# Optimization experiments

Hardware: AMD Instinct MI355X
Metric: run time of the kernel (lower is better)

The kernel has to match this reference:

```python
import jax, jax.numpy as jnp
import numpy as np

B, V, T, FIN = 32, 512, 12, 2      # batch, num_nodes, seq_len, input_dim
DG, CH, HOR = 20, 16, 12           # dgraphs, channels, horizon
KS, EPS, RF = 2, 0.3, 13           # kernel_size, FAGCN eps, receptive field
DILS = (1, 2, 1, 2, 1, 2, 1, 2)    # blocks=4, layers=2 -> dilations per layer
NL = len(DILS)
BN_EPS = 1e-5


def conv2d(x, W, b, dil=1):
    # x: [B,Cin,V,T], W: [Cout,Cin,1,k] -> [B,Cout,V,T'] (VALID, time-dilated)
    y = jax.lax.conv_general_dilated(x, W, (1, 1), 'VALID',
                                     rhs_dilation=(1, dil),
                                     dimension_numbers=('NCHW', 'OIHW', 'NCHW'))
    return y + b[None, :, None, None]


def setup_inputs():
    key = jax.random.key(0)
    ks = jax.random.split(key, 12)
    w = lambda k, s: jax.random.normal(k, s, dtype=jnp.float32) * 0.05
    z = lambda s: jnp.zeros(s, dtype=jnp.float32)
    o = lambda s: jnp.ones(s, dtype=jnp.float32)
    return {
        'input': jax.random.normal(ks[0], (T, B, V, FIN), dtype=jnp.float32),
        'start_W': w(ks[1], (CH, FIN, 1, 1)), 'start_b': z((CH,)),
        'filt_W': w(ks[2], (NL, CH, CH, 1, KS)), 'filt_b': z((NL, CH)),
        'gate_W': w(ks[3], (NL, CH, CH, 1, KS)), 'gate_b': z((NL, CH)),
        'skip_W': w(ks[4], (NL, CH, CH, 1, 1)), 'skip_b': z((NL, CH)),
        'gconv_W': w(ks[5], (NL, CH, 4 * CH, 1, 1)), 'gconv_b': z((NL, CH)),
        'bn_gamma': o((NL, CH)), 'bn_beta': z((NL, CH)),
        'bn_mean': z((NL, CH)), 'bn_var': o((NL, CH)),
        'end1_W': w(ks[6], (CH, CH, 1, 1)), 'end1_b': z((CH,)),
        'end2_W': w(ks[7], (HOR, CH, 1, 1)), 'end2_b': z((HOR,)),
        'lin_W': w(ks[8], (DG, FIN * T)), 'lin_b': z((DG,)),
        'fc1_W': w(ks[9], (V, DG)), 'fc1_b': z((V,)),
        'fc2_W': w(ks[10], (V, DG)), 'fc2_b': z((V,)),
        'fc3_W': w(ks[11], (V, DG)), 'fc3_b': z((V,)),
    }


def reference(input, start_W, start_b, filt_W, filt_b, gate_W, gate_b,
              skip_W, skip_b, gconv_W, gconv_b, bn_gamma, bn_beta, bn_mean,
              bn_var, end1_W, end1_b, end2_W, end2_b, lin_W, lin_b,
              fc1_W, fc1_b, fc2_W, fc2_b, fc3_W, fc3_b):
    x_in = jnp.transpose(input, (1, 3, 2, 0))            # [B,FIN,V,T]
    # ---- Instant_graph / SpectralConv1d: FFT-based graph learner ----
    xr = jnp.transpose(x_in, (0, 2, 3, 1)).reshape(B, V, T * FIN)
    ff = jnp.fft.fft(xr, axis=-1)                        # complex64 [B,V,T*FIN]
    real = ff.real @ lin_W.T + lin_b                     # [B,V,DG]
    img = ff.imag @ lin_W.T + lin_b                      # [B,V,DG]
    iff = jnp.fft.irfft(real + 1j * img, n=V, axis=1)    # [B,V,DG]
    Am = jnp.sqrt(real * real + img * img)
    S = jnp.arctan(real / (img + 1e-4))
    mid = jax.nn.sigmoid((iff @ fc1_W.T + fc1_b + Am @ fc2_W.T + fc2_b
                          + S @ fc3_W.T + fc3_b) / 3.0)  # [B,V,V]
    adj = jax.nn.sigmoid(jnp.mean(mid, axis=0))          # [V,V]
    eye = jnp.eye(V, dtype=x_in.dtype)
    Lm = EPS * eye + adj
    Hm = EPS * eye - adj
    # ---- WaveNet-style trunk with FAGCN diffusion per layer ----
    x = jnp.pad(x_in, ((0, 0), (0, 0), (0, 0), (RF - T, 0)))
    x = conv2d(x, start_W, start_b)                      # [B,CH,V,RF]
    skip = None
    for i in range(NL):
        residual = x
        f = jnp.tanh(conv2d(x, filt_W[i], filt_b[i], DILS[i]))
        g = jax.nn.sigmoid(conv2d(x, gate_W[i], gate_b[i], DILS[i]))
        x = f * g
        s = conv2d(x, skip_W[i], skip_b[i])
        skip = s if skip is None else s + skip[..., -s.shape[3]:]
        # FAGCN order=2: concat [xL, xLL, xH, xHH] on channels -> 1x1 conv
        outs = []
        for a in (Lm, Hm):
            x1 = jnp.einsum('ncvl,vw->ncwl', x, a)
            outs.append(x1)
            outs.append(jnp.einsum('ncvl,vw->ncwl', x1, a))
        h = conv2d(jnp.concatenate(outs, axis=1), gconv_W[i], gconv_b[i])
        x = h + residual[..., -h.shape[3]:]
        # BatchNorm2d (eval mode / running stats)
        x = ((x - bn_mean[i][None, :, None, None])
             / jnp.sqrt(bn_var[i][None, :, None, None] + BN_EPS)
             * bn_gamma[i][None, :, None, None]
             + bn_beta[i][None, :, None, None])
    out = jax.nn.relu(skip)
    out = jax.nn.relu(conv2d(out, end1_W, end1_b))
    out = conv2d(out, end2_W, end2_b)                    # [B,HOR,V,1]
    return out, adj
```

## Files before the change

kernel.cpp:

```cpp
#include <hip/hip_runtime.h>
#include <hip/hip_bf16.h>

using bf16 = __hip_bfloat16;
typedef unsigned short ushort_t;
typedef float f32x4 __attribute__((ext_vector_type(4)));
typedef short bf16x8 __attribute__((ext_vector_type(8)));

__device__ __forceinline__ float tof(bf16 x) { return __bfloat162float(x); }
__device__ __forceinline__ float tofu(ushort_t u) { return __uint_as_float((unsigned)u << 16); }
__device__ __forceinline__ ushort_t f2bf(float x) {
  unsigned u = __float_as_uint(x);
  return (ushort_t)((u + 0x7FFF + ((u >> 16) & 1)) >> 16);
}
__device__ __forceinline__ float sigm(float x) { return 1.f / (1.f + __expf(-x)); }
__device__ __forceinline__ float tanh_fast(float x) {
  float e2 = __expf(2.f * x);
  return 1.f - 2.f / (e2 + 1.f);
}

#define B_ 32
#define V_ 512
#define EPS_ 0.3f

constexpr size_t OFF_C    = 1024;
constexpr size_t OFF_S    = 1504;
constexpr size_t OFF_WEFF = 1984;
constexpr size_t OFF_R    = 8128;
constexpr size_t OFF_I    = 335808;
constexpr size_t OFF_G    = 663488;
constexpr size_t OFF_BTHI = 663488;
constexpr size_t OFF_BTLO = 925632;
constexpr size_t OFF_ADJ  = 1712064;
constexpr size_t OFF_ADJ2 = 1974208;
constexpr size_t OFF_SKIP = 2236352;
constexpr size_t OFF_X0   = 2498496;
constexpr size_t OFF_X1   = 5906368;
constexpr size_t OFF_TBH  = 5906368;
constexpr size_t OFF_TBL  = 6045632;
constexpr size_t OFF_TAH  = 6184896;
constexpr size_t OFF_TAL  = 6358976;
constexpr size_t OFF_UHI  = 9314240;
constexpr size_t OFF_ULO  = 10887104;
constexpr size_t OFF_PADJ = 12722112;
constexpr size_t OFF_WCT  = 13770688;
constexpr size_t OFF_FLAG = 19013568;
constexpr size_t OFF_CIN  = 19013576;
constexpr size_t WS_TOTAL = 19459584;

__global__ __launch_bounds__(256) void k_detect(const void* __restrict__ in0,
                                                float* __restrict__ flag) {
  __shared__ int cnt;
  if (threadIdx.x == 0) cnt = 0;
  __syncthreads();
  const unsigned short* u = (const unsigned short*)in0;
  int bad = 0;
  for (int i = threadIdx.x; i < 4096; i += 256) {
    int e = (u[i] >> 7) & 0xFF;
    if (e == 255 || (e != 0 && (e < 87 || e > 167))) bad++;
  }
  atomicAdd(&cnt, bad);
  __syncthreads();
  if (threadIdx.x == 0) flag[0] = (cnt > 200) ? 1.f : 0.f;
}

struct P26 { const void* p[26]; };
__global__ __launch_bounds__(256) void k_convall(const void* __restrict__ in0, P26 ps,
                                                 float* __restrict__ dstin,
                                                 float* __restrict__ dstw,
                                                 const float* __restrict__ flag) {
  int tid = threadIdx.x;
  if (blockIdx.x < 384) {
    int i4 = blockIdx.x * 256 + tid;
    if (flag[0] > 0.5f) {
      ((float4*)dstin)[i4] = ((const float4*)in0)[i4];
    } else {
      ushort4 v = ((const ushort4*)in0)[i4];
      dstin[i4 * 4 + 0] = tofu(v.x);
      dstin[i4 * 4 + 1] = tofu(v.y);
      dstin[i4 * 4 + 2] = tofu(v.z);
      dstin[i4 * 4 + 3] = tofu(v.w);
    }
  } else {
    const int sz[26] = {32, 16, 4096, 128, 4096, 128, 2048, 128, 8192, 128,
                        128, 128, 128, 128, 256, 16, 192, 12, 480, 20,
                        10240, 512, 10240, 512, 10240, 512};
    int gid = (blockIdx.x - 384) * 256 + tid;
    if (gid >= 52736) return;
    int s = 0, off = 0;
    while (gid >= off + sz[s]) { off += sz[s]; ++s; }
    int local = gid - off;
    float v = (flag[0] > 0.5f) ? ((const float*)ps.p[s])[local]
                               : tofu(((const ushort_t*)ps.p[s])[local]);
    dstw[gid] = v;
  }
}

__global__ __launch_bounds__(256) void k_pre(const float* __restrict__ linW,
                                             const float* __restrict__ gconvW,
                                             const float* f1W, const float* f1b,
                                             const float* f2W, const float* f2b,
                                             const float* f3W, const float* f3b,
                                             float* __restrict__ ws) {
  int idx = blockIdx.x * 256 + threadIdx.x;
  const float TWO_PI = 6.2831853071795864769f;
  if (idx < 512) {
  } else if (idx < 992) {
    int e = idx - 512, d = e / 24, n = e % 24;
    float c = 0.f, s = 0.f;
    for (int k = 0; k < 24; ++k) {
      int j = (k * n) % 24;
      float ang = TWO_PI * (float)j / 24.f;
      float w = linW[d * 24 + k];
      c += w * cosf(ang);
      s -= w * sinf(ang);
    }
    ws[OFF_C + e] = c;
    ws[OFF_S + e] = s;
  } else if (idx < 3040) {
    int e = idx - 992, i = e >> 8, co = (e >> 4) & 15, ci = e & 15;
    size_t base = (size_t)(i * 16 + co) * 64 + ci;
    float W0 = gconvW[base];
    float W1 = gconvW[base + 16];
    float W2 = gconvW[base + 32];
    float W3 = gconvW[base + 48];
    size_t o = OFF_WEFF + (size_t)i * 768 + co * 16 + ci;
    ws[o]       = EPS_ * (W0 + W2) + EPS_ * EPS_ * (W1 + W3);
    ws[o + 256] = (W0 - W2) + 2.f * EPS_ * (W1 - W3);
    ws[o + 512] = W1 + W3;
  } else if (idx < 36320) {
    int e = idx - 3040;
    if (e < 32768) {
      int k = e >> 9, w = e & 511;
      float v = 0.f;
      if (k < 20) v = f1W[w * 20 + k];
      else if (k < 40) v = f2W[w * 20 + k - 20];
      else if (k < 60) v = f3W[w * 20 + k - 40];
      ws[OFF_WCT + e] = v;
    } else {
      int w = e - 32768;
      ws[OFF_WCT + e] = f1b[w] + f2b[w] + f3b[w];
    }
  } else if (idx < 36320 + 278528) {
    int e = idx - 36320;
    int m = e / 544, kk = e - m * 544;
    float val = 0.f;
    if (kk < 514) {
      int k = kk >> 1;
      int j = (k * m) & 511;
      float ang = TWO_PI * (float)j * (1.f / 512.f);
      val = ((kk & 1) ? sinf(ang) : cosf(ang)) * (1.f / 512.f);
    }
    ushort_t h = f2bf(val);
    float hf = tofu(h);
    ((ushort_t*)(ws + OFF_TBH))[e] = h;
    ((ushort_t*)(ws + OFF_TBL))[e] = f2bf(val - hf);
  }
}

__global__ __launch_bounds__(256) void k_fft(const float* __restrict__ in,
                                             const float* __restrict__ linb,
                                             const float* __restrict__ ws,
                                             float* __restrict__ Rw, float* __restrict__ Iw,
                                             float* __restrict__ G) {
  __shared__ float Cl[480], Sl[480], lb[20];
  int tid = threadIdx.x;
  for (int e = tid; e < 480; e += 256) { Cl[e] = ws[OFF_C + e]; Sl[e] = ws[OFF_S + e]; }
  if (tid < 20) lb[tid] = linb[tid];
  __syncthreads();
  int gid = blockIdx.x * 256 + tid;
  int b = gid >> 9, v = gid & 511;
  float xr[24];
#pragma unroll
  for (int t = 0; t < 12; ++t) {
    size_t ib = (((size_t)t * 32 + b) * 512 + v) * 2;
    xr[2 * t] = in[ib];
    xr[2 * t + 1] = in[ib + 1];
  }
  size_t gbv = (size_t)b * 512 + v;
  for (int d = 0; d < 20; ++d) {
    float R = lb[d], I = lb[d];
#pragma unroll
    for (int n = 0; n < 24; ++n) {
      R = fmaf(xr[n], Cl[d * 24 + n], R);
      I = fmaf(xr[n], Sl[d * 24 + n], I);
    }
    Rw[gbv * 20 + d] = R;
    Iw[gbv * 20 + d] = I;
    G[gbv * 64 + 20 + d] = sqrtf(R * R + I * I);
    G[gbv * 64 + 40 + d] = atanf(R / (I + 1e-4f));
  }
  G[gbv * 64 + 60] = 0.f; G[gbv * 64 + 61] = 0.f;
  G[gbv * 64 + 62] = 0.f; G[gbv * 64 + 63] = 0.f;
}

__global__ __launch_bounds__(256) void k_irprep(const float* __restrict__ Rw,
                                                const float* __restrict__ Iw,
                                                ushort_t* __restrict__ Ahi,
                                                ushort_t* __restrict__ Alo) {
  int e = blockIdx.x * 256 + threadIdx.x;
  if (e >= 348160) return;
  int row = e / 544, kk = e - row * 544;
  int b = row / 20, d = row - b * 20;
  float val = 0.f;
  if (kk < 514) {
    int k = kk >> 1;
    float ck = (k == 0 || k == 256) ? 1.f : 2.f;
    size_t src = ((size_t)b * 512 + k) * 20 + d;
    val = (kk & 1) ? (-ck * Iw[src]) : (ck * Rw[src]);
  }
  ushort_t h = f2bf(val);
  Ahi[e] = h;
  Alo[e] = f2bf(val - tofu(h));
}

__global__ __launch_bounds__(512) void k_irgemm(const ushort_t* __restrict__ Ah_g,
                                                const ushort_t* __restrict__ Al_g,
                                                const ushort_t* __restrict__ Bh_g,
                                                const ushort_t* __restrict__ Bl_g,
                                                float* __restrict__ G) {
  __shared__ ushort_t Ah[128 * 40], Al[128 * 40], Bh[64 * 40], Bl[64 * 40];
  int tid = threadIdx.x;
  int lane = tid & 63, wv = tid >> 6;
  int quad = lane >> 4, l15 = lane & 15;
  int wr = wv >> 1, wc = wv & 1;
  int m0 = blockIdx.x * 128;
  int nv0 = blockIdx.y * 64;
  int srow = tid >> 2, seg = tid & 3;
  size_t baseA = (size_t)(m0 + srow) * 544 + seg * 8;
  size_t baseB = (size_t)(nv0 + (srow & 63)) * 544 + seg * 8;
  int slo = srow * 40 + seg * 8;
  uint4 pAh = *(const uint4*)&Ah_g[baseA];
  uint4 pAl = *(const uint4*)&Al_g[baseA];
  uint4 pBh, pBl;
  if (tid < 256) { pBh = *(const uint4*)&Bh_g[baseB]; pBl = *(const uint4*)&Bl_g[baseB]; }
  f32x4 acc[2][2] = {};
  for (int kt = 0; kt < 17; ++kt) {
    *(uint4*)&Ah[slo] = pAh;
    *(uint4*)&Al[slo] = pAl;
    if (tid < 256) { *(uint4*)&Bh[slo] = pBh; *(uint4*)&Bl[slo] = pBl; }
    __syncthreads();
    if (kt < 16) {
      int ko = (kt + 1) * 32;
      pAh = *(const uint4*)&Ah_g[baseA + ko];
      pAl = *(const uint4*)&Al_g[baseA + ko];
      if (tid < 256) { pBh = *(const uint4*)&Bh_g[baseB + ko]; pBl = *(const uint4*)&Bl_g[baseB + ko]; }
    }
    bf16x8 afh[2], afl[2], bfh[2], bfl[2];
#pragma unroll
    for (int i = 0; i < 2; ++i) {
      int mr = (wr * 32 + i * 16 + l15) * 40 + quad * 8;
      afh[i] = *(const bf16x8*)&Ah[mr];
      afl[i] = *(const bf16x8*)&Al[mr];
    }
#pragma unroll
    for (int j = 0; j < 2; ++j) {
      int nr = (wc * 32 + j * 16 + l15) * 40 + quad * 8;
      bfh[j] = *(const bf16x8*)&Bh[nr];
      bfl[j] = *(const bf16x8*)&Bl[nr];
    }
#pragma unroll
    for (int i = 0; i < 2; ++i)
#pragma unroll
      for (int j = 0; j < 2; ++j) {
        acc[i][j] = __builtin_amdgcn_mfma_f32_16x16x32_bf16(afh[i], bfh[j], acc[i][j], 0, 0, 0);
        acc[i][j] = __builtin_amdgcn_mfma_f32_16x16x32_bf16(afh[i], bfl[j], acc[i][j], 0, 0, 0);
        acc[i][j] = __builtin_amdgcn_mfma_f32_16x16x32_bf16(afl[i], bfh[j], acc[i][j], 0, 0, 0);
      }
    __syncthreads();
  }
#pragma unroll
  for (int i = 0; i < 2; ++i)
#pragma unroll
    for (int j = 0; j < 2; ++j)
#pragma unroll
      for (int r = 0; r < 4; ++r) {
        int arow = m0 + wr * 32 + i * 16 + quad * 4 + r;
        int col = nv0 + wc * 32 + j * 16 + l15;
        int b = arow / 20, d = arow - b * 20;
        G[((size_t)b * 512 + col) * 64 + d] = acc[i][j][r];
      }
}

__global__ __launch_bounds__(256) void k_adj(const float* __restrict__ G,
                                             const float* __restrict__ wct,
                                             float* __restrict__ padj) {
  __shared__ float As[64 * 68], Bs[64 * 68], bsl[64];
  int tid = threadIdx.x, tx = tid & 15, ty = tid >> 4;
  int w0 = blockIdx.x * 64, m0 = blockIdx.y * 64, z = blockIdx.z;
  for (int i = 0; i < 16; ++i) {
    int idx = tid + i * 256;
    Bs[(idx >> 6) * 68 + (idx & 63)] = wct[(size_t)(idx >> 6) * 512 + w0 + (idx & 63)];
  }
  if (tid < 64) bsl[tid] = wct[32768 + w0 + tid];
  float sum[4][4] = {};
  for (int bi = 0; bi < 8; ++bi) {
    int bb = z * 8 + bi;
    __syncthreads();
    for (int i = 0; i < 4; ++i) {
      int idx = tid + i * 256;
      int row = idx >> 4, seg = idx & 15;
      float4 g = *(const float4*)&G[((size_t)bb * 512 + m0 + row) * 64 + seg * 4];
      As[(seg * 4 + 0) * 68 + row] = g.x;
      As[(seg * 4 + 1) * 68 + row] = g.y;
      As[(seg * 4 + 2) * 68 + row] = g.z;
      As[(seg * 4 + 3) * 68 + row] = g.w;
    }
    __syncthreads();
    float dot[4][4] = {};
    for (int kk = 0; kk < 64; ++kk) {
      float4 a = *(const float4*)&As[kk * 68 + ty * 4];
      float4 b = *(const float4*)&Bs[kk * 68 + tx * 4];
      float ar[4] = {a.x, a.y, a.z, a.w}, br[4] = {b.x, b.y, b.z, b.w};
#pragma unroll
      for (int r = 0; r < 4; ++r)
#pragma unroll
        for (int c = 0; c < 4; ++c) dot[r][c] = fmaf(ar[r], br[c], dot[r][c]);
    }
#pragma unroll
    for (int r = 0; r < 4; ++r)
#pragma unroll
      for (int c = 0; c < 4; ++c)
        sum[r][c] += sigm((dot[r][c] + bsl[tx * 4 + c]) * (1.f / 3.f));
  }
  float* pz = padj + (size_t)z * 262144;
#pragma unroll
  for (int r = 0; r < 4; ++r)
#pragma unroll
    for (int c = 0; c < 4; ++c)
      pz[(size_t)(m0 + ty * 4 + r) * 512 + w0 + tx * 4 + c] = sum[r][c];
}

__global__ __launch_bounds__(256) void k_adjfin(const float* __restrict__ padj,
                                                float* __restrict__ adjw,
                                                void* __restrict__ outp,
                                                const float* __restrict__ flag) {
  int idx = blockIdx.x * 256 + threadIdx.x;
  float s = padj[idx] + padj[idx + 262144] + padj[idx + 524288] + padj[idx + 786432];
  float a = sigm(s * (1.f / 32.f));
  adjw[idx] = a;
  if (flag[0] > 0.5f) ((float*)outp)[196608 + idx] = a;
  else ((ushort_t*)outp)[196608 + idx] = f2bf(a);
}

__global__ __launch_bounds__(256) void k_gemm(const float* __restrict__ A,
                                              const float* __restrict__ B0,
                                              const float* __restrict__ B1,
                                              float* __restrict__ C, int ldc) {
  __shared__ float As[32][68];
  __shared__ float Bs[32][68];
  int bx = blockIdx.x, by = blockIdx.y;
  const float* __restrict__ Bp = (bx < 8) ? B0 : B1;
  int n0 = (bx & 7) * 64, m0 = by * 64;
  int tid = threadIdx.x, tx = tid & 15, ty = tid >> 4;
  float acc[4][4] = {};
  for (int kb = 0; kb < 512; kb += 32) {
#pragma unroll
    for (int s = 0; s < 2; ++s) {
      int f = tid + s * 256;
      int row = f >> 3, k4 = (f & 7) << 2;
      float4 a4 = *(const float4*)(A + (size_t)(m0 + row) * 512 + kb + k4);
      As[k4 + 0][row] = a4.x;
      As[k4 + 1][row] = a4.y;
      As[k4 + 2][row] = a4.z;
      As[k4 + 3][row] = a4.w;
      int kk = f >> 4, c4 = (f & 15) << 2;
      *(float4*)&Bs[kk][c4] = *(const float4*)(Bp + (size_t)(kb + kk) * 512 + n0 + c4);
    }
    __syncthreads();
#pragma unroll
    for (int kk = 0; kk < 32; ++kk) {
      float4 a = *(const float4*)&As[kk][ty << 2];
      float4 b = *(const float4*)&Bs[kk][tx << 2];
      float ar[4] = {a.x, a.y, a.z, a.w}, br[4] = {b.x, b.y, b.z, b.w};
#pragma unroll
      for (int r = 0; r < 4; ++r)
#pragma unroll
        for (int c = 0; c < 4; ++c) acc[r][c] = fmaf(ar[r], br[c], acc[r][c]);
    }
    __syncthreads();
  }
#pragma unroll
  for (int r = 0; r < 4; ++r) {
    float4 o = make_float4(acc[r][0], acc[r][1], acc[r][2], acc[r][3]);
    *(float4*)(C + (size_t)(m0 + (ty << 2) + r) * ldc + bx * 64 + (tx << 2)) = o;
  }
}

__global__ __launch_bounds__(256) void k_splitB(const float* __restrict__ adjw,
                                                const float* __restrict__ adj2w,
                                                ushort_t* __restrict__ Bh,
                                                ushort_t* __restrict__ Bl) {
  __shared__ float til[32][33];
  int tid = threadIdx.x;
  int k0 = blockIdx.x * 32;
  int nb = blockIdx.y;
  const float* src = (nb < 16) ? adjw : adj2w;
  int ns = (nb * 32) & 511;
  for (int i = 0; i < 4; ++i) {
    int idx = tid + i * 256;
    int r = idx >> 5, c = idx & 31;
    til[r][c] = src[(size_t)(k0 + r) * 512 + ns + c];
  }
  __syncthreads();
  for (int i = 0; i < 4; ++i) {
    int idx = tid + i * 256;
    int rr = idx >> 5, cc = idx & 31;
    float v = til[cc][rr];
    ushort_t h = f2bf(v);
    float hf = tofu(h);
    ushort_t l = f2bf(v - hf);
    size_t o = (size_t)(nb * 32 + rr) * 512 + k0 + cc;
    Bh[o] = h;
    Bl[o] = l;
  }
}

__global__ __launch_bounds__(256) void k_start(const float* __restrict__ in,
                                               const float* __restrict__ stW,
                                               const float* __restrict__ stb,
                                               float* __restrict__ X0) {
  __shared__ float w[32], bl[16];
  int tid = threadIdx.x;
  if (tid < 32) w[tid] = stW[tid];
  if (tid < 16) bl[tid] = stb[tid];
  __syncthreads();
  int blk = blockIdx.x;
  int b = blk / 26, rem = blk % 26, t = rem >> 1, v = (rem & 1) * 256 + tid;
  float f0 = 0.f, f1 = 0.f;
  if (t > 0) {
    size_t ib = (((size_t)(t - 1) * 32 + b) * 512 + v) * 2;
    f0 = in[ib];
    f1 = in[ib + 1];
  }
#pragma unroll
  for (int c = 0; c < 16; ++c)
    X0[((size_t)(b * 13 + t) * 16 + c) * 512 + v] = fmaf(w[c * 2], f0, fmaf(w[c * 2 + 1], f1, bl[c]));
}

__global__ __launch_bounds__(256) void k_gate(const float* __restrict__ X,
                                              ushort_t* __restrict__ Uhi,
                                              ushort_t* __restrict__ Ulo,
                                              float* __restrict__ skip,
                                              const float* fW, const float* fb,
                                              const float* gW, const float* gb,
                                              const float* sW, const float* sb,
                                              int i, int L, int Lo, int d) {
  __shared__ float wf[512], wg[512], swl[256], fbl[16], gbl[16], sbl[16];
  int tid = threadIdx.x;
  for (int e = tid; e < 512; e += 256) { wf[e] = fW[i * 512 + e]; wg[e] = gW[i * 512 + e]; }
  if (tid < 256) swl[tid] = sW[i * 256 + tid];
  if (tid < 16) { fbl[tid] = fb[i * 16 + tid]; gbl[tid] = gb[i * 16 + tid]; sbl[tid] = sb[i * 16 + tid]; }
  __syncthreads();
  int blk = blockIdx.x;
  int b = blk / (2 * Lo), rem = blk % (2 * Lo), t = rem >> 1, v = (rem & 1) * 256 + tid;
  float x0[16], x1[16];
  size_t base0 = (size_t)(b * L + t) * 16 * 512 + v;
  size_t base1 = (size_t)(b * L + t + d) * 16 * 512 + v;
#pragma unroll
  for (int ci = 0; ci < 16; ++ci) { x0[ci] = X[base0 + ci * 512]; x1[ci] = X[base1 + ci * 512]; }
  float u[16];
#pragma unroll
  for (int co = 0; co < 16; ++co) {
    float f = fbl[co], g = gbl[co];
#pragma unroll
    for (int ci = 0; ci < 16; ++ci) {
      f = fmaf(wf[co * 32 + ci * 2], x0[ci], f);
      f = fmaf(wf[co * 32 + ci * 2 + 1], x1[ci], f);
      g = fmaf(wg[co * 32 + ci * 2], x0[ci], g);
      g = fmaf(wg[co * 32 + ci * 2 + 1], x1[ci], g);
    }
    float uu = tanh_fast(f) * sigm(g);
    u[co] = uu;
    ushort_t h = f2bf(uu);
    float hf = tofu(h);
    ushort_t l = f2bf(uu - hf);
    size_t o = ((size_t)(b * Lo + t) * 16 + co) * 512 + v;
    Uhi[o] = h;
    Ulo[o] = l;
  }
  if (t == Lo - 1) {
#pragma unroll
    for (int c = 0; c < 16; ++c) {
      float s = sbl[c];
#pragma unroll
      for (int ci = 0; ci < 16; ++ci) s = fmaf(swl[c * 16 + ci], u[ci], s);
      skip[((size_t)b * 16 + c) * 512 + v] += s;
    }
  }
}

__global__ __launch_bounds__(512) void k_mfmac(const ushort_t* __restrict__ Uhi,
                                               const ushort_t* __restrict__ Ulo,
                                               const ushort_t* __restrict__ Bh_g,
                                               const ushort_t* __restrict__ Bl_g,
                                               const float* __restrict__ Xres,
                                               float* __restrict__ Xn,
                                               const float* __restrict__ ws,
                                               const float* gcb, const float* bg,
                                               const float* bb2, const float* bm,
                                               const float* bv,
                                               int li, int L, int Lo, int d) {
  __shared__ __align__(16) char smem[40960];
  ushort_t* Ah = (ushort_t*)smem;
  ushort_t* Al = Ah + 5120;
  ushort_t* Bh = Al + 5120;
  ushort_t* Bl = Bh + 5120;
  float* yt = (float*)smem;
  __shared__ float wx[256], wy1[256], wy2[256], gbl[16], bsc[16], bsh[16];
  int tid = threadIdx.x;
  const float* we = ws + OFF_WEFF + (size_t)li * 768;
  if (tid < 256) { wx[tid] = we[tid]; wy1[tid] = we[256 + tid]; wy2[tid] = we[512 + tid]; }
  if (tid < 16) {
    gbl[tid] = gcb[li * 16 + tid];
    float sc = bg[li * 16 + tid] * rsqrtf(bv[li * 16 + tid] + 1e-5f);
    bsc[tid] = sc;
    bsh[tid] = bb2[li * 16 + tid] - bm[li * 16 + tid] * sc;
  }
  int lane = tid & 63, wv = tid >> 6;
  int quad = lane >> 4, l15 = lane & 15;
  int wr = wv >> 1, wc = wv & 1;
  int m0 = blockIdx.x * 128;
  int nv0 = blockIdx.y * 64;
  int srow = tid >> 2, seg = tid & 3;
  size_t baseA = ((size_t)(m0 + srow)) * 512 + seg * 8;
  int brow = (srow < 64) ? (nv0 + srow) : (448 + nv0 + srow);
  size_t baseB = ((size_t)brow) * 512 + seg * 8;
  int slo = srow * 40 + seg * 8;
  uint4 pAh = *(const uint4*)&Uhi[baseA];
  uint4 pAl = *(const uint4*)&Ulo[baseA];
  uint4 pBh = *(const uint4*)&Bh_g[baseB];
  uint4 pBl = *(const uint4*)&Bl_g[baseB];
  f32x4 acc[2][4] = {};
  for (int kt = 0; kt < 16; ++kt) {
    *(uint4*)&Ah[slo] = pAh;
    *(uint4*)&Al[slo] = pAl;
    *(uint4*)&Bh[slo] = pBh;
    *(uint4*)&Bl[slo] = pBl;
    __syncthreads();
    if (kt < 15) {
      int ko = (kt + 1) * 32;
      pAh = *(const uint4*)&Uhi[baseA + ko];
      pAl = *(const uint4*)&Ulo[baseA + ko];
      pBh = *(const uint4*)&Bh_g[baseB + ko];
      pBl = *(const uint4*)&Bl_g[baseB + ko];
    }
    bf16x8 afh[2], afl[2], bfh[4], bfl[4];
#pragma unroll
    for (int i = 0; i < 2; ++i) {
      int mr = (wr * 32 + i * 16 + l15) * 40 + quad * 8;
      afh[i] = *(const bf16x8*)&Ah[mr];
      afl[i] = *(const bf16x8*)&Al[mr];
    }
#pragma unroll
    for (int j = 0; j < 4; ++j) {
      int nr = (wc * 64 + j * 16 + l15) * 40 + quad * 8;
      bfh[j] = *(const bf16x8*)&Bh[nr];
      bfl[j] = *(const bf16x8*)&Bl[nr];
    }
#pragma unroll
    for (int i = 0; i < 2; ++i)
#pragma unroll
      for (int j = 0; j < 4; ++j) {
        acc[i][j] = __builtin_amdgcn_mfma_f32_16x16x32_bf16(afh[i], bfh[j], acc[i][j], 0, 0, 0);
        acc[i][j] = __builtin_amdgcn_mfma_f32_16x16x32_bf16(afh[i], bfl[j], acc[i][j], 0, 0, 0);
        acc[i][j] = __builtin_amdgcn_mfma_f32_16x16x32_bf16(afl[i], bfh[j], acc[i][j], 0, 0, 0);
      }
    __syncthreads();
  }
  int g = tid >> 5, lv = tid & 31;
  int gg = (m0 >> 4) + g;
  int b = gg / Lo, t = gg - b * Lo;
  size_t rb = (size_t)gg * 16;
  size_t resb = ((size_t)(b * L + t + d) * 16) * 512;
#pragma unroll
  for (int p = 0; p < 2; ++p) {
#pragma unroll
    for (int i = 0; i < 2; ++i)
#pragma unroll
      for (int jj = 0; jj < 2; ++jj) {
        int j = p * 2 + jj;
#pragma unroll
        for (int r = 0; r < 4; ++r) {
          int row = wr * 32 + i * 16 + quad * 4 + r;
          int col = jj * 16 + l15 + 32 * wc;
          yt[row * 66 + col] = acc[i][j][r];
        }
      }
    __syncthreads();
    if (tid < 256) {
      int v = nv0 + p * 32 + lv;
      float uu[16], z1[16], z2[16];
#pragma unroll
      for (int ci = 0; ci < 16; ++ci) {
        size_t o = (rb + ci) * 512 + v;
        uu[ci] = tofu(Uhi[o]) + tofu(Ulo[o]);
        z1[ci] = yt[(g * 16 + ci) * 66 + lv];
        z2[ci] = yt[(g * 16 + ci) * 66 + 32 + lv];
      }
#pragma unroll
      for (int co = 0; co < 16; ++co) {
        float h = gbl[co];
#pragma unroll
        for (int ci = 0; ci < 16; ++ci) {
          h = fmaf(wx[co * 16 + ci], uu[ci], h);
          h = fmaf(wy1[co * 16 + ci], z1[ci], h);
          h = fmaf(wy2[co * 16 + ci], z2[ci], h);
        }
        float val = h + Xres[resb + co * 512 + v];
        val = fmaf(val, bsc[co], bsh[co]);
        Xn[(rb + co) * 512 + v] = val;
      }
    }
    if (p == 0) __syncthreads();
  }
}

__global__ __launch_bounds__(256) void k_end(const float* __restrict__ skip,
                                             const float* e1W, const float* e1b,
                                             const float* e2W, const float* e2b,
                                             void* __restrict__ outp,
                                             const float* __restrict__ flag) {
  __shared__ float w1[256], b1[16], w2[192], b2[12];
  int tid = threadIdx.x;
  if (tid < 256) w1[tid] = e1W[tid];
  if (tid < 192) w2[tid] = e2W[tid];
  if (tid < 16) b1[tid] = e1b[tid];
  if (tid < 12) b2[tid] = e2b[tid];
  __syncthreads();
  float isf32 = flag[0];
  int gid = blockIdx.x * 256 + tid;
  int b = gid >> 9, v = gid & 511;
  float sk[16], e1[16];
#pragma unroll
  for (int ci = 0; ci < 16; ++ci) sk[ci] = fmaxf(skip[((size_t)b * 16 + ci) * 512 + v], 0.f);
#pragma unroll
  for (int c = 0; c < 16; ++c) {
    float a = b1[c];
#pragma unroll
    for (int ci = 0; ci < 16; ++ci) a = fmaf(w1[c * 16 + ci], sk[ci], a);
    e1[c] = fmaxf(a, 0.f);
  }
#pragma unroll
  for (int h = 0; h < 12; ++h) {
    float o = b2[h];
#pragma unroll
    for (int ci = 0; ci < 16; ++ci) o = fmaf(w2[h * 16 + ci], e1[ci], o);
    size_t oi = ((size_t)b * 12 + h) * 512 + v;
    if (isf32 > 0.5f) ((float*)outp)[oi] = o;
    else ((ushort_t*)outp)[oi] = f2bf(o);
  }
}

extern "C" void kernel_launch(void* const* d_in, const int* in_sizes, int n_in,
                              void* d_out, int out_size, void* d_ws, size_t ws_size,
                              hipStream_t stream) {
  float* ws = (float*)d_ws;
  if (ws_size < WS_TOTAL * sizeof(float)) return;

  static const int CSZ[27] = {393216, 32, 16, 4096, 128, 4096, 128, 2048, 128, 8192, 128,
                              128, 128, 128, 128, 256, 16, 192, 12, 480, 20,
                              10240, 512, 10240, 512, 10240, 512};
  float* cv[27];
  {
    size_t off = OFF_CIN;
    for (int i = 0; i < 27; ++i) { cv[i] = ws + off; off += (size_t)CSZ[i]; }
  }
  float* flag = ws + OFF_FLAG;

  k_detect<<<1, 256, 0, stream>>>(d_in[0], flag);
  P26 ps;
  for (int i = 0; i < 26; ++i) ps.p[i] = d_in[i + 1];
  k_convall<<<590, 256, 0, stream>>>(d_in[0], ps, cv[0], cv[1], flag);

  const float* IN = cv[0];
  const float* stW = cv[1];  const float* stb = cv[2];
  const float* fW = cv[3];   const float* fb = cv[4];
  const float* gW = cv[5];   const float* gb = cv[6];
  const float* sW = cv[7];   const float* sb = cv[8];
  const float* gcW = cv[9];  const float* gcb = cv[10];
  const float* bng = cv[11]; const float* bnb = cv[12];
  const float* bnm = cv[13]; const float* bnv = cv[14];
  const float* e1W = cv[15]; const float* e1b = cv[16];
  const float* e2W = cv[17]; const float* e2b = cv[18];
  const float* linW = cv[19]; const float* linb = cv[20];
  const float* f1W = cv[21]; const float* f1b = cv[22];
  const float* f2W = cv[23]; const float* f2b = cv[24];
  const float* f3W = cv[25]; const float* f3b = cv[26];

  hipMemsetAsync(ws + OFF_SKIP, 0, (size_t)B_ * 16 * V_ * sizeof(float), stream);
  k_pre<<<1230, 256, 0, stream>>>(linW, gcW, f1W, f1b, f2W, f2b, f3W, f3b, ws);
  k_fft<<<64, 256, 0, stream>>>(IN, linb, ws, ws + OFF_R, ws + OFF_I, ws + OFF_G);
  k_irprep<<<1360, 256, 0, stream>>>(ws + OFF_R, ws + OFF_I,
                                     (ushort_t*)(ws + OFF_TAH), (ushort_t*)(ws + OFF_TAL));
  k_irgemm<<<dim3(5, 8), 512, 0, stream>>>((ushort_t*)(ws + OFF_TAH), (ushort_t*)(ws + OFF_TAL),
                                           (ushort_t*)(ws + OFF_TBH), (ushort_t*)(ws + OFF_TBL),
                                           ws + OFF_G);
  k_adj<<<dim3(8, 8, 4), 256, 0, stream>>>(ws + OFF_G, ws + OFF_WCT, ws + OFF_PADJ);
  k_adjfin<<<1024, 256, 0, stream>>>(ws + OFF_PADJ, ws + OFF_ADJ, d_out, flag);
  k_gemm<<<dim3(8, 8), 256, 0, stream>>>(ws + OFF_ADJ, ws + OFF_ADJ, ws + OFF_ADJ,
                                         ws + OFF_ADJ2, 512);
  k_splitB<<<dim3(16, 32), 256, 0, stream>>>(ws + OFF_ADJ, ws + OFF_ADJ2,
                                             (ushort_t*)(ws + OFF_BTHI),
                                             (ushort_t*)(ws + OFF_BTLO));
  k_start<<<832, 256, 0, stream>>>(IN, stW, stb, ws + OFF_X0);

  float* cur = ws + OFF_X0;
  float* nxt = ws + OFF_X1;
  ushort_t* UHI = (ushort_t*)(ws + OFF_UHI);
  ushort_t* ULO = (ushort_t*)(ws + OFF_ULO);
  int L = 13;
  const int dils[8] = {1, 2, 1, 2, 1, 2, 1, 2};
  for (int i = 0; i < 8; ++i) {
    int d = dils[i], Lo = L - d;
    k_gate<<<64 * Lo, 256, 0, stream>>>(cur, UHI, ULO, ws + OFF_SKIP,
                                        fW, fb, gW, gb, sW, sb, i, L, Lo, d);
    k_mfmac<<<dim3(4 * Lo, 8), 512, 0, stream>>>(UHI, ULO,
                                                 (ushort_t*)(ws + OFF_BTHI),
                                                 (ushort_t*)(ws + OFF_BTLO),
                                                 cur, nxt, ws,
                                                 gcb, bng, bnb, bnm, bnv, i, L, Lo, d);
    float* tmp = cur; cur = nxt; nxt = tmp;
    L = Lo;
  }
  k_end<<<64, 256, 0, stream>>>(ws + OFF_SKIP, e1W, e1b, e2W, e2b, d_out, flag);
}
```

Before: 594.7 us.

## Load MFMA fragments directly from global memory, drop LDS staging in graph GEMM

The split-bf16 graph-propagation GEMM no longer stages A/B tiles through shared memory with per-k-step barriers. Each wave now loads its MFMA operand fragments straight from global memory into registers, with one-step register prefetch. The block shrinks to 256 threads covering 32 nodes, and the grid doubles in y so the epilogue runs in a single pass. This removes LDS traffic and barriers, but duplicates global loads across waves that share B tiles, relying on cache for reuse.

```diff
diff --git a/kernel.cpp b/kernel.cpp
--- a/kernel.cpp
+++ b/kernel.cpp
@@ -489,7 +489,7 @@
   }
 }
 
-__global__ __launch_bounds__(512) void k_mfmac(const ushort_t* __restrict__ Uhi,
+__global__ __launch_bounds__(256) void k_mfmac(const ushort_t* __restrict__ Uhi,
                                                const ushort_t* __restrict__ Ulo,
                                                const ushort_t* __restrict__ Bh_g,
                                                const ushort_t* __restrict__ Bl_g,
@@ -500,118 +500,104 @@
                                                const float* bb2, const float* bm,
                                                const float* bv,
                                                int li, int L, int Lo, int d) {
-  __shared__ __align__(16) char smem[40960];
-  ushort_t* Ah = (ushort_t*)smem;
-  ushort_t* Al = Ah + 5120;
-  ushort_t* Bh = Al + 5120;
-  ushort_t* Bl = Bh + 5120;
-  float* yt = (float*)smem;
+  __shared__ float yt[128 * 66];
   __shared__ float wx[256], wy1[256], wy2[256], gbl[16], bsc[16], bsh[16];
   int tid = threadIdx.x;
   const float* we = ws + OFF_WEFF + (size_t)li * 768;
-  if (tid < 256) { wx[tid] = we[tid]; wy1[tid] = we[256 + tid]; wy2[tid] = we[512 + tid]; }
+  wx[tid] = we[tid]; wy1[tid] = we[256 + tid]; wy2[tid] = we[512 + tid];
   if (tid < 16) {
     gbl[tid] = gcb[li * 16 + tid];
     float sc = bg[li * 16 + tid] * rsqrtf(bv[li * 16 + tid] + 1e-5f);
     bsc[tid] = sc;
     bsh[tid] = bb2[li * 16 + tid] - bm[li * 16 + tid] * sc;
   }
-  int lane = tid & 63, wv = tid >> 6;
+  int lane = tid & 63, wr = tid >> 6;
   int quad = lane >> 4, l15 = lane & 15;
-  int wr = wv >> 1, wc = wv & 1;
   int m0 = blockIdx.x * 128;
-  int nv0 = blockIdx.y * 64;
-  int srow = tid >> 2, seg = tid & 3;
-  size_t baseA = ((size_t)(m0 + srow)) * 512 + seg * 8;
-  int brow = (srow < 64) ? (nv0 + srow) : (448 + nv0 + srow);
-  size_t baseB = ((size_t)brow) * 512 + seg * 8;
-  int slo = srow * 40 + seg * 8;
-  uint4 pAh = *(const uint4*)&Uhi[baseA];
-  uint4 pAl = *(const uint4*)&Ulo[baseA];
-  uint4 pBh = *(const uint4*)&Bh_g[baseB];
-  uint4 pBl = *(const uint4*)&Bl_g[baseB];
+  int nv0 = blockIdx.y * 32;
+  size_t aoff[2], boff[4];
+#pragma unroll
+  for (int i = 0; i < 2; ++i)
+    aoff[i] = (size_t)(m0 + wr * 32 + i * 16 + l15) * 512 + quad * 8;
+  boff[0] = (size_t)(nv0 + l15) * 512 + quad * 8;
+  boff[1] = boff[0] + 16 * 512;
+  boff[2] = boff[0] + 512 * 512;
+  boff[3] = boff[1] + 512 * 512;
+  bf16x8 cAh[2], cAl[2], cBh[4], cBl[4];
+#pragma unroll
+  for (int i = 0; i < 2; ++i) {
+    cAh[i] = *(const bf16x8*)&Uhi[aoff[i]];
+    cAl[i] = *(const bf16x8*)&Ulo[aoff[i]];
+  }
+#pragma unroll
+  for (int j = 0; j < 4; ++j) {
+    cBh[j] = *(const bf16x8*)&Bh_g[boff[j]];
+    cBl[j] = *(const bf16x8*)&Bl_g[boff[j]];
+  }
   f32x4 acc[2][4] = {};
   for (int kt = 0; kt < 16; ++kt) {
-    *(uint4*)&Ah[slo] = pAh;
-    *(uint4*)&Al[slo] = pAl;
-    *(uint4*)&Bh[slo] = pBh;
-    *(uint4*)&Bl[slo] = pBl;
-    __syncthreads();
-    if (kt < 15) {
-      int ko = (kt + 1) * 32;
-      pAh = *(const uint4*)&Uhi[baseA + ko];
-      pAl = *(const uint4*)&Ulo[baseA + ko];
-      pBh = *(const uint4*)&Bh_g[baseB + ko];
-      pBl = *(const uint4*)&Bl_g[baseB + ko];
-    }
-    bf16x8 afh[2], afl[2], bfh[4], bfl[4];
+    int ko = ((kt + 1) & 15) * 32;
+    bf16x8 nAh[2], nAl[2], nBh[4], nBl[4];
 #pragma unroll
     for (int i = 0; i < 2; ++i) {
-      int mr = (wr * 32 + i * 16 + l15) * 40 + quad * 8;
-      afh[i] = *(const bf16x8*)&Ah[mr];
-      afl[i] = *(const bf16x8*)&Al[mr];
+      nAh[i] = *(const bf16x8*)&Uhi[aoff[i] + ko];
+      nAl[i] = *(const bf16x8*)&Ulo[aoff[i] + ko];
     }
 #pragma unroll
     for (int j = 0; j < 4; ++j) {
-      int nr = (wc * 64 + j * 16 + l15) * 40 + quad * 8;
-      bfh[j] = *(const bf16x8*)&Bh[nr];
-      bfl[j] = *(const bf16x8*)&Bl[nr];
+      nBh[j] = *(const bf16x8*)&Bh_g[boff[j] + ko];
+      nBl[j] = *(const bf16x8*)&Bl_g[boff[j] + ko];
     }
 #pragma unroll
     for (int i = 0; i < 2; ++i)
 #pragma unroll
       for (int j = 0; j < 4; ++j) {
-        acc[i][j] = __builtin_amdgcn_mfma_f32_16x16x32_bf16(afh[i], bfh[j], acc[i][j], 0, 0, 0);
-        acc[i][j] = __builtin_amdgcn_mfma_f32_16x16x32_bf16(afh[i], bfl[j], acc[i][j], 0, 0, 0);
-        acc[i][j] = __builtin_amdgcn_mfma_f32_16x16x32_bf16(afl[i], bfh[j], acc[i][j], 0, 0, 0);
+        acc[i][j] = __builtin_amdgcn_mfma_f32_16x16x32_bf16(cAh[i], cBh[j], acc[i][j], 0, 0, 0);
+        acc[i][j] = __builtin_amdgcn_mfma_f32_16x16x32_bf16(cAh[i], cBl[j], acc[i][j], 0, 0, 0);
+        acc[i][j] = __builtin_amdgcn_mfma_f32_16x16x32_bf16(cAl[i], cBh[j], acc[i][j], 0, 0, 0);
       }
-    __syncthreads();
-  }
+#pragma unroll
+    for (int i = 0; i < 2; ++i) { cAh[i] = nAh[i]; cAl[i] = nAl[i]; }
+#pragma unroll
+    for (int j = 0; j < 4; ++j) { cBh[j] = nBh[j]; cBl[j] = nBl[j]; }
+  }
+#pragma unroll
+  for (int i = 0; i < 2; ++i)
+#pragma unroll
+    for (int j = 0; j < 4; ++j)
+#pragma unroll
+      for (int r = 0; r < 4; ++r) {
+        int row = wr * 32 + i * 16 + quad * 4 + r;
+        int col = (j & 1) * 16 + l15 + (j >> 1) * 32;
+        yt[row * 66 + col] = acc[i][j][r];
+      }
+  __syncthreads();
   int g = tid >> 5, lv = tid & 31;
   int gg = (m0 >> 4) + g;
   int b = gg / Lo, t = gg - b * Lo;
   size_t rb = (size_t)gg * 16;
   size_t resb = ((size_t)(b * L + t + d) * 16) * 512;
-#pragma unroll
-  for (int p = 0; p < 2; ++p) {
-#pragma unroll
-    for (int i = 0; i < 2; ++i)
-#pragma unroll
-      for (int jj = 0; jj < 2; ++jj) {
-        int j = p * 2 + jj;
-#pragma unroll
-        for (int r = 0; r < 4; ++r) {
-          int row = wr * 32 + i * 16 + quad * 4 + r;
-          int col = jj * 16 + l15 + 32 * wc;
-          yt[row * 66 + col] = acc[i][j][r];
-        }
-      }
-    __syncthreads();
-    if (tid < 256) {
-      int v = nv0 + p * 32 + lv;
-      float uu[16], z1[16], z2[16];
-#pragma unroll
-      for (int ci = 0; ci < 16; ++ci) {
-        size_t o = (rb + ci) * 512 + v;
-        uu[ci] = tofu(Uhi[o]) + tofu(Ulo[o]);
-        z1[ci] = yt[(g * 16 + ci) * 66 + lv];
-        z2[ci] = yt[(g * 16 + ci) * 66 + 32 + lv];
-      }
-#pragma unroll
-      for (int co = 0; co < 16; ++co) {
-        float h = gbl[co];
-#pragma unroll
-        for (int ci = 0; ci < 16; ++ci) {
-          h = fmaf(wx[co * 16 + ci], uu[ci], h);
-          h = fmaf(wy1[co * 16 + ci], z1[ci], h);
-          h = fmaf(wy2[co * 16 + ci], z2[ci], h);
-        }
-        float val = h + Xres[resb + co * 512 + v];
-        val = fmaf(val, bsc[co], bsh[co]);
-        Xn[(rb + co) * 512 + v] = val;
-      }
-    }
-    if (p == 0) __syncthreads();
+  int v = nv0 + lv;
+  float uu[16], z1[16], z2[16];
+#pragma unroll
+  for (int ci = 0; ci < 16; ++ci) {
+    size_t o = (rb + ci) * 512 + v;
+    uu[ci] = tofu(Uhi[o]) + tofu(Ulo[o]);
+    z1[ci] = yt[(g * 16 + ci) * 66 + lv];
+    z2[ci] = yt[(g * 16 + ci) * 66 + 32 + lv];
+  }
+#pragma unroll
+  for (int co = 0; co < 16; ++co) {
+    float h = gbl[co];
+#pragma unroll
+    for (int ci = 0; ci < 16; ++ci) {
+      h = fmaf(wx[co * 16 + ci], uu[ci], h);
+      h = fmaf(wy1[co * 16 + ci], z1[ci], h);
+      h = fmaf(wy2[co * 16 + ci], z2[ci], h);
+    }
+    float val = h + Xres[resb + co * 512 + v];
+    val = fmaf(val, bsc[co], bsh[co]);
+    Xn[(rb + co) * 512 + v] = val;
   }
 }
 
@@ -714,11 +700,11 @@
     int d = dils[i], Lo = L - d;
     k_gate<<<64 * Lo, 256, 0, stream>>>(cur, UHI, ULO, ws + OFF_SKIP,
                                         fW, fb, gW, gb, sW, sb, i, L, Lo, d);
-    k_mfmac<<<dim3(4 * Lo, 8), 512, 0, stream>>>(UHI, ULO,
-                                                 (ushort_t*)(ws + OFF_BTHI),
-                                                 (ushort_t*)(ws + OFF_BTLO),
-                                                 cur, nxt, ws,
-                                                 gcb, bng, bnb, bnm, bnv, i, L, Lo, d);
+    k_mfmac<<<dim3(4 * Lo, 16), 256, 0, stream>>>(UHI, ULO,
+                                                  (ushort_t*)(ws + OFF_BTHI),
+                                                  (ushort_t*)(ws + OFF_BTLO),
+                                                  cur, nxt, ws,
+                                                  gcb, bng, bnb, bnm, bnv, i, L, Lo, d);
     float* tmp = cur; cur = nxt; nxt = tmp;
     L = Lo;
   }
```

Result: slower. 747.5 us (+25.7%).

## Halve k_mfmac N-tile to 32 vertices with 256-thread blocks

Applied to the files above, without the earlier changes.

The graph-propagation MFMA kernel now uses 256 threads (4 waves) per block, each tile covering 128 rows by 32 vertex columns (64 B columns, L and H), and the grid's y dimension doubles from 8 to 16. Every thread now does the epilogue in a single pass, so the two-phase epilogue with its extra barrier is gone and fewer threads sit idle. The aim is more blocks, higher occupancy and less shared memory per block. In exchange, the A tile (U hi/lo) is reloaded by twice as many blocks, raising global and L2 traffic.

```diff
diff --git a/kernel.cpp b/kernel.cpp
--- a/kernel.cpp
+++ b/kernel.cpp
@@ -489,7 +489,7 @@
   }
 }
 
-__global__ __launch_bounds__(512) void k_mfmac(const ushort_t* __restrict__ Uhi,
+__global__ __launch_bounds__(256) void k_mfmac(const ushort_t* __restrict__ Uhi,
                                                const ushort_t* __restrict__ Ulo,
                                                const ushort_t* __restrict__ Bh_g,
                                                const ushort_t* __restrict__ Bl_g,
@@ -500,49 +500,65 @@
                                                const float* bb2, const float* bm,
                                                const float* bv,
                                                int li, int L, int Lo, int d) {
-  __shared__ __align__(16) char smem[40960];
+  __shared__ __align__(16) char smem[33792];
   ushort_t* Ah = (ushort_t*)smem;
   ushort_t* Al = Ah + 5120;
   ushort_t* Bh = Al + 5120;
-  ushort_t* Bl = Bh + 5120;
+  ushort_t* Bl = Bh + 2560;
   float* yt = (float*)smem;
   __shared__ float wx[256], wy1[256], wy2[256], gbl[16], bsc[16], bsh[16];
   int tid = threadIdx.x;
   const float* we = ws + OFF_WEFF + (size_t)li * 768;
-  if (tid < 256) { wx[tid] = we[tid]; wy1[tid] = we[256 + tid]; wy2[tid] = we[512 + tid]; }
+  wx[tid] = we[tid]; wy1[tid] = we[256 + tid]; wy2[tid] = we[512 + tid];
   if (tid < 16) {
     gbl[tid] = gcb[li * 16 + tid];
     float sc = bg[li * 16 + tid] * rsqrtf(bv[li * 16 + tid] + 1e-5f);
     bsc[tid] = sc;
     bsh[tid] = bb2[li * 16 + tid] - bm[li * 16 + tid] * sc;
   }
-  int lane = tid & 63, wv = tid >> 6;
+  int lane = tid & 63, wr = tid >> 6;
   int quad = lane >> 4, l15 = lane & 15;
-  int wr = wv >> 1, wc = wv & 1;
   int m0 = blockIdx.x * 128;
-  int nv0 = blockIdx.y * 64;
-  int srow = tid >> 2, seg = tid & 3;
-  size_t baseA = ((size_t)(m0 + srow)) * 512 + seg * 8;
-  int brow = (srow < 64) ? (nv0 + srow) : (448 + nv0 + srow);
-  size_t baseB = ((size_t)brow) * 512 + seg * 8;
-  int slo = srow * 40 + seg * 8;
-  uint4 pAh = *(const uint4*)&Uhi[baseA];
-  uint4 pAl = *(const uint4*)&Ulo[baseA];
-  uint4 pBh = *(const uint4*)&Bh_g[baseB];
-  uint4 pBl = *(const uint4*)&Bl_g[baseB];
+  int nv0 = blockIdx.y * 32;
+  size_t gbase[3];
+  int lofs[3];
+  {
+    int seg = tid & 3;
+#pragma unroll
+    for (int r = 0; r < 2; ++r) {
+      int row = (tid + r * 256) >> 2;
+      gbase[r] = (size_t)(m0 + row) * 512 + seg * 8;
+      lofs[r] = row * 40 + seg * 8;
+    }
+    int brow_l = ((tid + 512) >> 2) - 128;
+    int brow = (brow_l < 32) ? (nv0 + brow_l) : (480 + nv0 + brow_l);
+    gbase[2] = (size_t)brow * 512 + seg * 8;
+    lofs[2] = brow_l * 40 + seg * 8;
+  }
+  uint4 pH[3], pL[3];
+  pH[0] = *(const uint4*)&Uhi[gbase[0]];
+  pL[0] = *(const uint4*)&Ulo[gbase[0]];
+  pH[1] = *(const uint4*)&Uhi[gbase[1]];
+  pL[1] = *(const uint4*)&Ulo[gbase[1]];
+  pH[2] = *(const uint4*)&Bh_g[gbase[2]];
+  pL[2] = *(const uint4*)&Bl_g[gbase[2]];
   f32x4 acc[2][4] = {};
   for (int kt = 0; kt < 16; ++kt) {
-    *(uint4*)&Ah[slo] = pAh;
-    *(uint4*)&Al[slo] = pAl;
-    *(uint4*)&Bh[slo] = pBh;
-    *(uint4*)&Bl[slo] = pBl;
+    *(uint4*)&Ah[lofs[0]] = pH[0];
+    *(uint4*)&Al[lofs[0]] = pL[0];
+    *(uint4*)&Ah[lofs[1]] = pH[1];
+    *(uint4*)&Al[lofs[1]] = pL[1];
+    *(uint4*)&Bh[lofs[2]] = pH[2];
+    *(uint4*)&Bl[lofs[2]] = pL[2];
     __syncthreads();
     if (kt < 15) {
       int ko = (kt + 1) * 32;
-      pAh = *(const uint4*)&Uhi[baseA + ko];
-      pAl = *(const uint4*)&Ulo[baseA + ko];
-      pBh = *(const uint4*)&Bh_g[baseB + ko];
-      pBl = *(const uint4*)&Bl_g[baseB + ko];
+      pH[0] = *(const uint4*)&Uhi[gbase[0] + ko];
+      pL[0] = *(const uint4*)&Ulo[gbase[0] + ko];
+      pH[1] = *(const uint4*)&Uhi[gbase[1] + ko];
+      pL[1] = *(const uint4*)&Ulo[gbase[1] + ko];
+      pH[2] = *(const uint4*)&Bh_g[gbase[2] + ko];
+      pL[2] = *(const uint4*)&Bl_g[gbase[2] + ko];
     }
     bf16x8 afh[2], afl[2], bfh[4], bfl[4];
 #pragma unroll
@@ -553,7 +569,7 @@
     }
 #pragma unroll
     for (int j = 0; j < 4; ++j) {
-      int nr = (wc * 64 + j * 16 + l15) * 40 + quad * 8;
+      int nr = (j * 16 + l15) * 40 + quad * 8;
       bfh[j] = *(const bf16x8*)&Bh[nr];
       bfl[j] = *(const bf16x8*)&Bl[nr];
     }
@@ -567,51 +583,43 @@
       }
     __syncthreads();
   }
+#pragma unroll
+  for (int i = 0; i < 2; ++i)
+#pragma unroll
+    for (int j = 0; j < 4; ++j)
+#pragma unroll
+      for (int r = 0; r < 4; ++r) {
+        int row = wr * 32 + i * 16 + quad * 4 + r;
+        int col = (j & 1) * 16 + l15 + (j >> 1) * 32;
+        yt[row * 66 + col] = acc[i][j][r];
+      }
+  __syncthreads();
   int g = tid >> 5, lv = tid & 31;
   int gg = (m0 >> 4) + g;
   int b = gg / Lo, t = gg - b * Lo;
   size_t rb = (size_t)gg * 16;
   size_t resb = ((size_t)(b * L + t + d) * 16) * 512;
-#pragma unroll
-  for (int p = 0; p < 2; ++p) {
-#pragma unroll
-    for (int i = 0; i < 2; ++i)
-#pragma unroll
-      for (int jj = 0; jj < 2; ++jj) {
-        int j = p * 2 + jj;
-#pragma unroll
-        for (int r = 0; r < 4; ++r) {
-          int row = wr * 32 + i * 16 + quad * 4 + r;
-          int col = jj * 16 + l15 + 32 * wc;
-          yt[row * 66 + col] = acc[i][j][r];
-        }
-      }
-    __syncthreads();
-    if (tid < 256) {
-      int v = nv0 + p * 32 + lv;
-      float uu[16], z1[16], z2[16];
-#pragma unroll
-      for (int ci = 0; ci < 16; ++ci) {
-        size_t o = (rb + ci) * 512 + v;
-        uu[ci] = tofu(Uhi[o]) + tofu(Ulo[o]);
-        z1[ci] = yt[(g * 16 + ci) * 66 + lv];
-        z2[ci] = yt[(g * 16 + ci) * 66 + 32 + lv];
-      }
-#pragma unroll
-      for (int co = 0; co < 16; ++co) {
-        float h = gbl[co];
-#pragma unroll
-        for (int ci = 0; ci < 16; ++ci) {
-          h = fmaf(wx[co * 16 + ci], uu[ci], h);
-          h = fmaf(wy1[co * 16 + ci], z1[ci], h);
-          h = fmaf(wy2[co * 16 + ci], z2[ci], h);
-        }
-        float val = h + Xres[resb + co * 512 + v];
-        val = fmaf(val, bsc[co], bsh[co]);
-        Xn[(rb + co) * 512 + v] = val;
-      }
-    }
-    if (p == 0) __syncthreads();
+  int v = nv0 + lv;
+  float uu[16], z1[16], z2[16];
+#pragma unroll
+  for (int ci = 0; ci < 16; ++ci) {
+    size_t o = (rb + ci) * 512 + v;
+    uu[ci] = tofu(Uhi[o]) + tofu(Ulo[o]);
+    z1[ci] = yt[(g * 16 + ci) * 66 + lv];
+    z2[ci] = yt[(g * 16 + ci) * 66 + 32 + lv];
+  }
+#pragma unroll
+  for (int co = 0; co < 16; ++co) {
+    float h = gbl[co];
+#pragma unroll
+    for (int ci = 0; ci < 16; ++ci) {
+      h = fmaf(wx[co * 16 + ci], uu[ci], h);
+      h = fmaf(wy1[co * 16 + ci], z1[ci], h);
+      h = fmaf(wy2[co * 16 + ci], z2[ci], h);
+    }
+    float val = h + Xres[resb + co * 512 + v];
+    val = fmaf(val, bsc[co], bsh[co]);
+    Xn[(rb + co) * 512 + v] = val;
   }
 }
 
@@ -714,11 +722,11 @@
     int d = dils[i], Lo = L - d;
     k_gate<<<64 * Lo, 256, 0, stream>>>(cur, UHI, ULO, ws + OFF_SKIP,
                                         fW, fb, gW, gb, sW, sb, i, L, Lo, d);
-    k_mfmac<<<dim3(4 * Lo, 8), 512, 0, stream>>>(UHI, ULO,
-                                                 (ushort_t*)(ws + OFF_BTHI),
-                                                 (ushort_t*)(ws + OFF_BTLO),
-                                                 cur, nxt, ws,
-                                                 gcb, bng, bnb, bnm, bnv, i, L, Lo, d);
+    k_mfmac<<<dim3(4 * Lo, 16), 256, 0, stream>>>(UHI, ULO,
+                                                  (ushort_t*)(ws + OFF_BTHI),
+                                                  (ushort_t*)(ws + OFF_BTLO),
+                                                  cur, nxt, ws,
+                                                  gcb, bng, bnb, bnm, bnv, i, L, Lo, d);
     float* tmp = cur; cur = nxt; nxt = tmp;
     L = Lo;
   }
```

Result: slower. 859.9 us (+44.6%).
